# Performance work log

Measured on AMD Instinct MI355X. Metric: run time of the kernel, lower is better.

## Reference

```python
import jax, jax.numpy as jnp
import numpy as np
from jax import lax

DIM = 256
HEADS = 8
DIM_HEAD = 32
INNER = HEADS * DIM_HEAD  # 256
SCALE = DIM_HEAD ** -0.5
EPS = 1e-5
DN = ('NCHW', 'OIHW', 'NCHW')


def chan_layer_norm(x, g):
    # LayerNorm over channel dim (axis=1), biased variance
    mean = jnp.mean(x, axis=1, keepdims=True)
    var = jnp.mean((x - mean) ** 2, axis=1, keepdims=True)
    return (x - mean) / jnp.sqrt(var + EPS) * g


def conv1x1(x, w):
    return lax.conv_general_dilated(x, w, (1, 1), 'VALID', dimension_numbers=DN)


def dwconv3x3(x, w):
    # depthwise 3x3, padding=1, groups=channels; w: [C,1,3,3]
    return lax.conv_general_dilated(x, w, (1, 1), 'SAME', dimension_numbers=DN,
                                    feature_group_count=x.shape[1])


def setup_inputs() -> dict:
    key = jax.random.key(0)
    ks = jax.random.split(key, 9)
    B, X, Y = 16, 64, 64
    fmap = jax.random.normal(ks[0], (B, DIM, X, Y), dtype=jnp.float32)
    w = lambda k, shape: (jax.random.normal(k, shape, dtype=jnp.float32) * 0.02)
    return {
        'fmap': fmap,
        'g_norm': jnp.ones((1, DIM, 1, 1), dtype=jnp.float32),
        'wq1': w(ks[1], (INNER, DIM, 1, 1)),
        'wq_dw': w(ks[2], (INNER, 1, 3, 3)),
        'wk1': w(ks[3], (INNER, DIM, 1, 1)),
        'wk_dw': w(ks[4], (INNER, 1, 3, 3)),
        'wv1': w(ks[5], (INNER, DIM, 1, 1)),
        'wv_dw': w(ks[6], (INNER, 1, 3, 3)),
        'wo': w(ks[7], (DIM, INNER, 1, 1)),
        'g_out': jnp.ones((1, DIM, 1, 1), dtype=jnp.float32),
    }


def reference(fmap, g_norm, wq1, wq_dw, wk1, wk_dw, wv1, wv_dw, wo, g_out):
    b, _, X, Y = fmap.shape
    n = X * Y
    x = chan_layer_norm(fmap, g_norm)
    # QKV: 1x1 conv -> depthwise 3x3 conv (dropout is identity in eval)
    q = dwconv3x3(conv1x1(x, wq1), wq_dw)
    k = dwconv3x3(conv1x1(x, wk1), wk_dw)
    v = dwconv3x3(conv1x1(x, wv1), wv_dw)
    # b (h c) x y -> b h n c
    def split(t):
        return t.reshape(b, HEADS, DIM_HEAD, n).transpose(0, 1, 3, 2)
    q, k, v = split(q), split(k), split(v)
    q = jax.nn.softmax(q, axis=-1) * SCALE   # softmax over feature dim
    k = jax.nn.softmax(k, axis=-2)           # softmax over sequence dim
    ctx = jnp.einsum('bhnd,bhne->bhde', k, v)    # [b,h,d,d]
    out = jnp.einsum('bhnd,bhde->bhne', q, ctx)  # [b,h,n,d]
    # b h n d -> b (h d) x y
    out = out.transpose(0, 1, 3, 2).reshape(b, INNER, X, Y)
    out = jax.nn.silu(out)
    out = conv1x1(out, wo)
    return chan_layer_norm(out, g_out)
```

## Files before the change

### kernel.cpp

```cpp
#include <hip/hip_runtime.h>


typedef unsigned short u16;
typedef __bf16 bf16x8 __attribute__((ext_vector_type(8)));
typedef float f32x4 __attribute__((ext_vector_type(4)));
typedef float f32x16 __attribute__((ext_vector_type(16)));

#define DEV static __device__ __forceinline__

DEV float b2f(u16 u) { return __uint_as_float(((unsigned int)u) << 16); }
DEV u16 f2bf(float f) {
  unsigned int u = __float_as_uint(f);
  return (u16)((u + 0x7fffu + ((u >> 16) & 1u)) >> 16);
}
DEV void gl2lds16(const void* g, void* l) {
  __builtin_amdgcn_global_load_lds((__attribute__((address_space(1))) void*)g,
                                   (__attribute__((address_space(3))) void*)l, 16, 0, 0);
}

__global__ __launch_bounds__(256) void prep_kernel(const float* __restrict__ wk,
                                                   const float* __restrict__ wv,
                                                   const float* __restrict__ wq,
                                                   const float* __restrict__ wo,
                                                   u16* __restrict__ wb) {
  const int i = blockIdx.x * 256 + threadIdx.x;
  const float* src = (blockIdx.y == 0) ? wk : (blockIdx.y == 1) ? wv : (blockIdx.y == 2) ? wq : wo;
  wb[blockIdx.y * 65536 + i] = f2bf(src[i]);
}

__global__ __launch_bounds__(256) void ln_tin_kernel(const float* __restrict__ f,
                                                     const float* __restrict__ g,
                                                     u16* __restrict__ xT) {
  __shared__ u16 tile[64 * 258];
  __shared__ float red[2 * 256];
  __shared__ float mu_s[64], inv_s[64];
  const int t = threadIdx.x;
  const int p0 = blockIdx.x * 64;
  const int b = blockIdx.y;
  const long fb = (long)b * 256 * 4096;
  const int p = t & 63, cg = t >> 6;
  float s1 = 0.f, s2 = 0.f;
  for (int pass = 0; pass < 64; ++pass) {
    int c = pass * 4 + cg;
    float v = f[fb + (long)c * 4096 + p0 + p];
    s1 += v; s2 += v * v;
    tile[p * 258 + c] = f2bf(v);
  }
  red[cg * 64 + p] = s1;
  red[256 + cg * 64 + p] = s2;
  __syncthreads();
  if (t < 64) {
    float a1 = red[t] + red[64 + t] + red[128 + t] + red[192 + t];
    float a2 = red[256 + t] + red[320 + t] + red[384 + t] + red[448 + t];
    float mu = a1 * (1.f / 256.f);
    float var = a2 * (1.f / 256.f) - mu * mu;
    mu_s[t] = mu;
    inv_s[t] = 1.0f / sqrtf(var + 1e-5f);
  }
  __syncthreads();
  {
    float gc = g[t];
    for (int pp = 0; pp < 64; ++pp) {
      float v = b2f(tile[pp * 258 + t]);
      xT[((long)b * 4096 + p0 + pp) * 256 + t] = f2bf((v - mu_s[pp]) * inv_s[pp] * gc);
    }
  }
}

__global__ __launch_bounds__(256) void gemm_bt_kernel(
    const u16* __restrict__ A, const u16* __restrict__ B0, const u16* __restrict__ B1,
    u16* __restrict__ Cg, int ldc, long sA, long sC) {
  __shared__ u16 As[128 * 32];
  __shared__ u16 Bs[128 * 32];
  const int t = threadIdx.x;
  const int wave = t >> 6, lane = t & 63, quad = lane >> 4, l16 = lane & 15;
  const int wr = wave >> 1, wc = wave & 1;
  const int m0 = blockIdx.x * 128;
  const int jt = blockIdx.y;
  const int b = blockIdx.z;
  const u16* Ab = A + (long)b * sA + (long)m0 * 256;
  const u16* Bt = (jt < 2 ? B0 : B1) + (jt & 1) * 128 * 256;
  u16* Cb = Cg + (long)b * sC + (long)m0 * ldc + jt * 128;

  const int srow = lane >> 2;
  const int scol = (lane & 3) * 8;
  f32x4 acc[4][4];
#pragma unroll
  for (int i = 0; i < 4; ++i)
#pragma unroll
    for (int j = 0; j < 4; ++j) acc[i][j] = (f32x4){0.f, 0.f, 0.f, 0.f};

  const int aoff = (wr * 64 + l16) * 32 + quad * 8;
  const int boff = (wc * 64 + l16) * 32 + quad * 8;

  for (int ks = 0; ks < 8; ++ks) {
    const int k0 = ks * 32;
    __syncthreads();
    for (int i = wave; i < 8; i += 4) {
      gl2lds16(Ab + (i * 16 + srow) * 256 + k0 + scol, &As[i * 512 + lane * 8]);
      gl2lds16(Bt + (i * 16 + srow) * 256 + k0 + scol, &Bs[i * 512 + lane * 8]);
    }
    __syncthreads();
    bf16x8 af[4], bfr[4];
#pragma unroll
    for (int mt = 0; mt < 4; ++mt) af[mt] = *(const bf16x8*)&As[aoff + mt * 512];
#pragma unroll
    for (int nt = 0; nt < 4; ++nt) bfr[nt] = *(const bf16x8*)&Bs[boff + nt * 512];
#pragma unroll
    for (int mt = 0; mt < 4; ++mt)
#pragma unroll
      for (int nt = 0; nt < 4; ++nt)
        acc[mt][nt] = __builtin_amdgcn_mfma_f32_16x16x32_bf16(af[mt], bfr[nt], acc[mt][nt], 0, 0, 0);
  }
#pragma unroll
  for (int mt = 0; mt < 4; ++mt) {
    const int mbase = wr * 64 + mt * 16 + quad * 4;
#pragma unroll
    for (int nt = 0; nt < 4; ++nt) {
      const int n = wc * 64 + nt * 16 + l16;
#pragma unroll
      for (int r = 0; r < 4; ++r)
        Cb[(long)(mbase + r) * ldc + n] = f2bf(acc[mt][nt][r]);
    }
  }
}

__global__ __launch_bounds__(256) void dwq_kernel(const u16* __restrict__ qT,
                                                  const float* __restrict__ wdw,
                                                  u16* __restrict__ qp) {
  const int t = threadIdx.x;
  const int strip = blockIdx.x, h = blockIdx.y, b = blockIdx.z;
  const int x0 = strip * 4;
  const int wave = t >> 6, lane = t & 63;
  const int ysel = lane & 15, cg = lane >> 4;
  const int y = wave * 16 + ysel;
  float w[72];
#pragma unroll
  for (int q = 0; q < 8; ++q)
#pragma unroll
    for (int i = 0; i < 9; ++i) w[q * 9 + i] = wdw[(h * 32 + cg * 8 + q) * 9 + i];
  const u16* qb = qT + (long)b * 4096 * 256 + h * 32 + cg * 8;
  u16* ob = qp + ((long)b * 4096 + y) * 256 + h * 32 + cg * 8;

#pragma unroll
  for (int it = 0; it < 4; ++it) {
    const int x = x0 + it;
    float acc[8] = {0.f, 0.f, 0.f, 0.f, 0.f, 0.f, 0.f, 0.f};
#pragma unroll
    for (int r = 0; r < 3; ++r) {
      const int xx = x - 1 + r;
#pragma unroll
      for (int dy = 0; dy < 3; ++dy) {
        const int yy = y - 1 + dy;
        if (((unsigned)xx < 64u) & ((unsigned)yy < 64u)) {
          uint4 pk = *(const uint4*)(qb + (long)(xx * 64 + yy) * 256);
          const u16* s = (const u16*)&pk;
#pragma unroll
          for (int q = 0; q < 8; ++q)
            acc[q] = fmaf(w[q * 9 + r * 3 + dy], b2f(s[q]), acc[q]);
        }
      }
    }
    float e[8];
    float s = 0.f;
#pragma unroll
    for (int q = 0; q < 8; ++q) { e[q] = __expf(acc[q]); s += e[q]; }
    s += __shfl_xor(s, 16);
    s += __shfl_xor(s, 32);
    const float inv = 0.17677669529663687f / s;
    uint4 o;
    u16* os = (u16*)&o;
#pragma unroll
    for (int q = 0; q < 8; ++q) os[q] = f2bf(e[q] * inv);
    *(uint4*)(ob + (long)x * 16384) = o;
  }
}

__global__ __launch_bounds__(1024, 4) void ctx_kernel(const u16* __restrict__ kvT,
                                                      const float* __restrict__ wkdw,
                                                      const float* __restrict__ wvdw,
                                                      float* __restrict__ par0,
                                                      float* __restrict__ par1) {
  __shared__ float redb[8 * 1088];
  __shared__ float redk[16 * 32];
  const int t = threadIdx.x;
  const int strip = blockIdx.x, h = blockIdx.y, b = blockIdx.z;
  const int wave = t >> 6, lane = t & 63;
  const int g = wave >> 2, wq = wave & 3;
  const int x0 = strip * 32 + g * 8;
  const int c = lane & 31, half = lane >> 5;
  const int ystart = wq * 16 + half * 8;
  float wk[9], wv[9];
#pragma unroll
  for (int i = 0; i < 9; ++i) {
    wk[i] = wkdw[(h * 32 + c) * 9 + i];
    wv[i] = wvdw[(h * 32 + c) * 9 + i];
  }
  const u16* kb = kvT + (long)b * 4096 * 512 + h * 32 + c;

  float fk[3][10], fv[3][10];
#pragma unroll
  for (int r = 0; r < 2; ++r) {
    const int x = x0 - 1 + r;
#pragma unroll
    for (int m = 0; m < 10; ++m) {
      const int yy = ystart - 1 + m;
      float a = 0.f, bb = 0.f;
      if (((unsigned)x < 64u) & ((unsigned)yy < 64u)) {
        const u16* p = kb + (long)(x * 64 + yy) * 512;
        a = b2f(p[0]);
        bb = b2f(p[256]);
      }
      fk[r][m] = a; fv[r][m] = bb;
    }
  }
  f32x16 acc;
#pragma unroll
  for (int r = 0; r < 16; ++r) acc[r] = 0.f;
  float ks = 0.f;

  for (int it = 0; it < 8; ++it) {
    const int x = x0 + it;
    {
      const int xn = x + 1;
#pragma unroll
      for (int m = 0; m < 10; ++m) {
        const int yy = ystart - 1 + m;
        float a = 0.f, bb = 0.f;
        if (((unsigned)xn < 64u) & ((unsigned)yy < 64u)) {
          const u16* p = kb + (long)(xn * 64 + yy) * 512;
          a = b2f(p[0]);
          bb = b2f(p[256]);
        }
        fk[2][m] = a; fv[2][m] = bb;
      }
    }
    union { bf16x8 v; u16 s[8]; } af, bf_;
#pragma unroll
    for (int j = 0; j < 8; ++j) {
      float a = 0.f, bb = 0.f;
#pragma unroll
      for (int r = 0; r < 3; ++r)
#pragma unroll
        for (int dy = 0; dy < 3; ++dy) {
          a = fmaf(wk[r * 3 + dy], fk[r][j + dy], a);
          bb = fmaf(wv[r * 3 + dy], fv[r][j + dy], bb);
        }
      const u16 eb = f2bf(__expf(a));
      ks += b2f(eb);
      af.s[j] = eb;
      bf_.s[j] = f2bf(bb);
    }
    acc = __builtin_amdgcn_mfma_f32_32x32x16_bf16(af.v, bf_.v, acc, 0, 0, 0);
#pragma unroll
    for (int m = 0; m < 10; ++m) {
      fk[0][m] = fk[1][m]; fk[1][m] = fk[2][m];
      fv[0][m] = fv[1][m]; fv[1][m] = fv[2][m];
    }
  }
  ks += __shfl_xor(ks, 32);
  if (half == 0) redk[wave * 32 + c] = ks;
  if (wave >= 8) {
#pragma unroll
    for (int r = 0; r < 16; ++r) redb[(wave - 8) * 1088 + lane * 17 + r] = acc[r];
  }
  __syncthreads();
  if (wave < 8) {
#pragma unroll
    for (int r = 0; r < 16; ++r) acc[r] += redb[wave * 1088 + lane * 17 + r];
  }
  __syncthreads();
  if (wave >= 4 && wave < 8) {
#pragma unroll
    for (int r = 0; r < 16; ++r) redb[(wave - 4) * 1088 + lane * 17 + r] = acc[r];
  }
  __syncthreads();
  if (wave < 4) {
#pragma unroll
    for (int r = 0; r < 16; ++r) acc[r] += redb[wave * 1088 + lane * 17 + r];
  }
  __syncthreads();
  if (wave >= 1 && wave < 4) {
#pragma unroll
    for (int r = 0; r < 16; ++r) redb[(wave - 1) * 1088 + lane * 17 + r] = acc[r];
  }
  __syncthreads();
  if (wave == 0) {
    float* par = (strip ? par1 : par0) + (long)(b * 8 + h) * 1056;
#pragma unroll
    for (int r = 0; r < 16; ++r) {
      float sum = acc[r] + redb[lane * 17 + r] + redb[1088 + lane * 17 + r] +
                  redb[2176 + lane * 17 + r];
      const int d = (r & 3) + 8 * (r >> 2) + 4 * half;
      par[d * 32 + c] = sum;
    }
    if (t < 32) {
      float s = 0.f;
#pragma unroll
      for (int w = 0; w < 16; ++w) s += redk[w * 32 + t];
      par[1024 + t] = s;
    }
  }
}

__global__ __launch_bounds__(256) void reduce_kernel(const float* __restrict__ par0,
                                                     const float* __restrict__ par1,
                                                     float* __restrict__ ctxF,
                                                     float* __restrict__ ksF) {
  const int bh = blockIdx.x;
  const long base = (long)bh * 1056;
  for (int i = threadIdx.x; i < 1056; i += 256) {
    float v = par0[base + i] + par1[base + i];
    if (i < 1024) ctxF[(long)bh * 1024 + i] = v;
    else ksF[(long)bh * 32 + (i - 1024)] = v;
  }
}

__global__ __launch_bounds__(256) void attn_kernel(const u16* __restrict__ qp,
                                                   const float* __restrict__ ctxg,
                                                   const float* __restrict__ ksumg,
                                                   u16* __restrict__ sout) {
  __shared__ u16 cnhi[8 * 32 * 40];
  __shared__ u16 cnlo[8 * 32 * 40];
  const int t = threadIdx.x;
  const int p0 = blockIdx.x * 128;
  const int b = blockIdx.y;
  const int wave = t >> 6, lane = t & 63, quad = lane >> 4, l16 = lane & 15;

  for (int j = 0; j < 32; ++j) {
    const int idx = j * 256 + t;
    const int e = idx & 31, d = (idx >> 5) & 31, h = idx >> 10;
    const float c = ctxg[(long)b * 8192 + idx] / ksumg[(long)b * 256 + (idx >> 5)];
    const u16 hi = f2bf(c);
    cnhi[h * 1280 + e * 40 + d] = hi;
    cnlo[h * 1280 + e * 40 + d] = f2bf(c - b2f(hi));
  }
  __syncthreads();

  const u16* qb = qp + ((long)b * 4096 + p0 + wave * 32) * 256;
  u16* ob = sout + ((long)b * 4096 + p0 + wave * 32) * 256;
#pragma unroll
  for (int h = 0; h < 8; ++h) {
    const int cb = h * 1280 + quad * 8;
    const bf16x8 bhi0 = *(const bf16x8*)&cnhi[cb + l16 * 40];
    const bf16x8 bhi1 = *(const bf16x8*)&cnhi[cb + (16 + l16) * 40];
    const bf16x8 blo0 = *(const bf16x8*)&cnlo[cb + l16 * 40];
    const bf16x8 blo1 = *(const bf16x8*)&cnlo[cb + (16 + l16) * 40];
#pragma unroll
    for (int rt = 0; rt < 2; ++rt) {
      const bf16x8 af = *(const bf16x8*)&qb[(rt * 16 + l16) * 256 + h * 32 + quad * 8];
      f32x4 a0 = (f32x4){0.f, 0.f, 0.f, 0.f};
      f32x4 a1 = (f32x4){0.f, 0.f, 0.f, 0.f};
      a0 = __builtin_amdgcn_mfma_f32_16x16x32_bf16(af, blo0, a0, 0, 0, 0);
      a0 = __builtin_amdgcn_mfma_f32_16x16x32_bf16(af, bhi0, a0, 0, 0, 0);
      a1 = __builtin_amdgcn_mfma_f32_16x16x32_bf16(af, blo1, a1, 0, 0, 0);
      a1 = __builtin_amdgcn_mfma_f32_16x16x32_bf16(af, bhi1, a1, 0, 0, 0);
#pragma unroll
      for (int r = 0; r < 4; ++r) {
        const int row = rt * 16 + quad * 4 + r;
        const float v0 = a0[r], v1 = a1[r];
        ob[(long)row * 256 + h * 32 + l16] = f2bf(v0 / (1.f + __expf(-v0)));
        ob[(long)row * 256 + h * 32 + 16 + l16] = f2bf(v1 / (1.f + __expf(-v1)));
      }
    }
  }
}

__global__ __launch_bounds__(256) void ln_tout_kernel(const u16* __restrict__ y,
                                                      const float* __restrict__ gout,
                                                      float* __restrict__ out) {
  __shared__ u16 tile[64 * 258];
  __shared__ float red[2 * 256];
  __shared__ float mu_s[64], inv_s[64];
  const int t = threadIdx.x;
  const int p0 = blockIdx.x * 64;
  const int b = blockIdx.y;
  for (int p = 0; p < 64; ++p)
    tile[p * 258 + t] = y[((long)b * 4096 + p0 + p) * 256 + t];
  __syncthreads();
  {
    const int p = t & 63, part = t >> 6;
    float s1 = 0.f, s2 = 0.f;
    for (int k = 0; k < 64; ++k) {
      float v = b2f(tile[p * 258 + part * 64 + k]);
      s1 += v; s2 += v * v;
    }
    red[part * 64 + p] = s1;
    red[256 + part * 64 + p] = s2;
  }
  __syncthreads();
  if (t < 64) {
    float s1 = red[t] + red[64 + t] + red[128 + t] + red[192 + t];
    float s2 = red[256 + t] + red[320 + t] + red[384 + t] + red[448 + t];
    float mu = s1 * (1.f / 256.f);
    float var = s2 * (1.f / 256.f) - mu * mu;
    mu_s[t] = mu;
    inv_s[t] = 1.0f / sqrtf(var + 1e-5f);
  }
  __syncthreads();
  {
    const int p = t & 63, cg = t >> 6;
    const long ob = (long)b * 256 * 4096;
    for (int pass = 0; pass < 64; ++pass) {
      int c = pass * 4 + cg;
      float v = b2f(tile[p * 258 + c]);
      out[ob + (long)c * 4096 + p0 + p] = (v - mu_s[p]) * inv_s[p] * gout[c];
    }
  }
}

extern "C" void kernel_launch(void* const* d_in, const int* in_sizes, int n_in,
                              void* d_out, int out_size, void* d_ws, size_t ws_size,
                              hipStream_t stream) {
  (void)in_sizes; (void)n_in; (void)out_size; (void)ws_size;
  const float* fmap = (const float*)d_in[0];
  const float* gnorm = (const float*)d_in[1];
  const float* wq1 = (const float*)d_in[2];
  const float* wqdw = (const float*)d_in[3];
  const float* wk1 = (const float*)d_in[4];
  const float* wkdw = (const float*)d_in[5];
  const float* wv1 = (const float*)d_in[6];
  const float* wvdw = (const float*)d_in[7];
  const float* wo = (const float*)d_in[8];
  const float* gout = (const float*)d_in[9];
  float* out = (float*)d_out;
  char* ws = (char*)d_ws;

  float* par0 = (float*)(ws);
  u16* wb = (u16*)(ws + 540672);
  float* par1 = (float*)(ws + 1064960);
  u16* wk_bf = wb;
  u16* wv_bf = wb + 65536;
  u16* wq_bf = wb + 131072;
  u16* wo_bf = wb + 196608;
  u16* xT = (u16*)(ws + 2097152);
  u16* kvT = (u16*)(ws + 35651584);
  u16* qT = kvT;
  float* ctxF = (float*)(ws + 35651584);
  float* ksF = (float*)(ws + 35651584 + 524288);
  u16* qp = (u16*)(ws + 69206016);
  u16* sbuf = xT;
  u16* ybuf = qp;

  prep_kernel<<<dim3(256, 4), 256, 0, stream>>>(wk1, wv1, wq1, wo, wb);
  ln_tin_kernel<<<dim3(64, 16), 256, 0, stream>>>(fmap, gnorm, xT);
  gemm_bt_kernel<<<dim3(32, 4, 16), 256, 0, stream>>>(xT, wk_bf, wv_bf, kvT, 512,
                                                      4096L * 256, 4096L * 512);
  ctx_kernel<<<dim3(2, 8, 16), 1024, 0, stream>>>(kvT, wkdw, wvdw, par0, par1);
  gemm_bt_kernel<<<dim3(32, 2, 16), 256, 0, stream>>>(xT, wq_bf, wq_bf, qT, 256,
                                                      4096L * 256, 4096L * 256);
  dwq_kernel<<<dim3(16, 8, 16), 256, 0, stream>>>(qT, wqdw, qp);
  reduce_kernel<<<dim3(128), 256, 0, stream>>>(par0, par1, ctxF, ksF);
  attn_kernel<<<dim3(32, 16), 256, 0, stream>>>(qp, ctxF, ksF, sbuf);
  gemm_bt_kernel<<<dim3(32, 2, 16), 256, 0, stream>>>(sbuf, wo_bf, wo_bf, ybuf, 256,
                                                      4096L * 256, 4096L * 256);
  ln_tout_kernel<<<dim3(64, 16), 256, 0, stream>>>(ybuf, gout, out);
}
```

Measured before the change: 327.9 us.

## Interleave K/V channels, stage dwq halo tile in LDS, split attn by head pairs

The K and V projection weights are interleaved row-wise so the GEMM writes K and V channels side by side. This lets ctx_kernel fetch both with a single 32-bit load instead of two strided 16-bit loads. dwq_kernel now stages a 6-row halo tile of q in shared memory, so the 3x3 stencil reads LDS rather than issuing nine bounds-checked global loads per output. attn_kernel gains a grid dimension over head pairs, which cuts per-block LDS and context setup and increases the block count, at the cost of re-reading q rows in smaller per-head slices.

```diff
diff --git a/kernel.cpp b/kernel.cpp
--- a/kernel.cpp
+++ b/kernel.cpp
@@ -24,8 +24,11 @@
                                                    const float* __restrict__ wo,
                                                    u16* __restrict__ wb) {
   const int i = blockIdx.x * 256 + threadIdx.x;
-  const float* src = (blockIdx.y == 0) ? wk : (blockIdx.y == 1) ? wv : (blockIdx.y == 2) ? wq : wo;
-  wb[blockIdx.y * 65536 + i] = f2bf(src[i]);
+  const int yb = blockIdx.y;
+  if (yb == 0)      wb[(i >> 8) * 512 + (i & 255)] = f2bf(wk[i]);
+  else if (yb == 1) wb[(i >> 8) * 512 + 256 + (i & 255)] = f2bf(wv[i]);
+  else if (yb == 2) wb[131072 + i] = f2bf(wq[i]);
+  else              wb[196608 + i] = f2bf(wo[i]);
 }
 
 __global__ __launch_bounds__(256) void ln_tin_kernel(const float* __restrict__ f,
@@ -128,37 +131,48 @@
 __global__ __launch_bounds__(256) void dwq_kernel(const u16* __restrict__ qT,
                                                   const float* __restrict__ wdw,
                                                   u16* __restrict__ qp) {
+  __shared__ u16 tile[6 * 66 * 40];
   const int t = threadIdx.x;
   const int strip = blockIdx.x, h = blockIdx.y, b = blockIdx.z;
   const int x0 = strip * 4;
   const int wave = t >> 6, lane = t & 63;
   const int ysel = lane & 15, cg = lane >> 4;
   const int y = wave * 16 + ysel;
+  const int ty = t >> 2, tc = t & 3;
+
+  if (t < 48) {
+    const int slot = t >> 3, brd = (t >> 2) & 1, c4 = t & 3;
+    *(uint4*)&tile[slot * 2640 + (brd ? 65 * 40 : 0) + c4 * 8] = (uint4){0, 0, 0, 0};
+  }
+  const u16* qrow = qT + (long)b * 4096 * 256 + h * 32 + tc * 8;
+#pragma unroll
+  for (int s = 0; s < 6; ++s) {
+    const int xx = x0 - 1 + s;
+    uint4 v = (uint4){0, 0, 0, 0};
+    if ((unsigned)xx < 64u) v = *(const uint4*)(qrow + (long)(xx * 64 + ty) * 256);
+    *(uint4*)&tile[s * 2640 + (ty + 1) * 40 + tc * 8] = v;
+  }
   float w[72];
 #pragma unroll
   for (int q = 0; q < 8; ++q)
 #pragma unroll
     for (int i = 0; i < 9; ++i) w[q * 9 + i] = wdw[(h * 32 + cg * 8 + q) * 9 + i];
-  const u16* qb = qT + (long)b * 4096 * 256 + h * 32 + cg * 8;
+  __syncthreads();
+
   u16* ob = qp + ((long)b * 4096 + y) * 256 + h * 32 + cg * 8;
-
 #pragma unroll
   for (int it = 0; it < 4; ++it) {
     const int x = x0 + it;
     float acc[8] = {0.f, 0.f, 0.f, 0.f, 0.f, 0.f, 0.f, 0.f};
 #pragma unroll
     for (int r = 0; r < 3; ++r) {
-      const int xx = x - 1 + r;
 #pragma unroll
       for (int dy = 0; dy < 3; ++dy) {
-        const int yy = y - 1 + dy;
-        if (((unsigned)xx < 64u) & ((unsigned)yy < 64u)) {
-          uint4 pk = *(const uint4*)(qb + (long)(xx * 64 + yy) * 256);
-          const u16* s = (const u16*)&pk;
-#pragma unroll
-          for (int q = 0; q < 8; ++q)
-            acc[q] = fmaf(w[q * 9 + r * 3 + dy], b2f(s[q]), acc[q]);
-        }
+        uint4 pk = *(const uint4*)&tile[(it + r) * 2640 + (y + dy) * 40 + cg * 8];
+        const u16* s = (const u16*)&pk;
+#pragma unroll
+        for (int q = 0; q < 8; ++q)
+          acc[q] = fmaf(w[q * 9 + r * 3 + dy], b2f(s[q]), acc[q]);
       }
     }
     float e[8];
@@ -196,7 +210,7 @@
     wk[i] = wkdw[(h * 32 + c) * 9 + i];
     wv[i] = wvdw[(h * 32 + c) * 9 + i];
   }
-  const u16* kb = kvT + (long)b * 4096 * 512 + h * 32 + c;
+  const u16* kb = kvT + (long)b * 4096 * 512 + 2 * (h * 32 + c);
 
   float fk[3][10], fv[3][10];
 #pragma unroll
@@ -207,9 +221,9 @@
       const int yy = ystart - 1 + m;
       float a = 0.f, bb = 0.f;
       if (((unsigned)x < 64u) & ((unsigned)yy < 64u)) {
-        const u16* p = kb + (long)(x * 64 + yy) * 512;
-        a = b2f(p[0]);
-        bb = b2f(p[256]);
+        const unsigned u = *(const unsigned*)(kb + (long)(x * 64 + yy) * 512);
+        a = b2f((u16)(u & 0xffffu));
+        bb = b2f((u16)(u >> 16));
       }
       fk[r][m] = a; fv[r][m] = bb;
     }
@@ -228,9 +242,9 @@
         const int yy = ystart - 1 + m;
         float a = 0.f, bb = 0.f;
         if (((unsigned)xn < 64u) & ((unsigned)yy < 64u)) {
-          const u16* p = kb + (long)(xn * 64 + yy) * 512;
-          a = b2f(p[0]);
-          bb = b2f(p[256]);
+          const unsigned u = *(const unsigned*)(kb + (long)(xn * 64 + yy) * 512);
+          a = b2f((u16)(u & 0xffffu));
+          bb = b2f((u16)(u >> 16));
         }
         fk[2][m] = a; fv[2][m] = bb;
       }
@@ -320,28 +334,31 @@
                                                    const float* __restrict__ ctxg,
                                                    const float* __restrict__ ksumg,
                                                    u16* __restrict__ sout) {
-  __shared__ u16 cnhi[8 * 32 * 40];
-  __shared__ u16 cnlo[8 * 32 * 40];
+  __shared__ u16 cnhi[2 * 32 * 40];
+  __shared__ u16 cnlo[2 * 32 * 40];
   const int t = threadIdx.x;
   const int p0 = blockIdx.x * 128;
-  const int b = blockIdx.y;
+  const int hp = blockIdx.y;
+  const int b = blockIdx.z;
   const int wave = t >> 6, lane = t & 63, quad = lane >> 4, l16 = lane & 15;
 
-  for (int j = 0; j < 32; ++j) {
-    const int idx = j * 256 + t;
-    const int e = idx & 31, d = (idx >> 5) & 31, h = idx >> 10;
-    const float c = ctxg[(long)b * 8192 + idx] / ksumg[(long)b * 256 + (idx >> 5)];
+  for (int j = 0; j < 8; ++j) {
+    const int lidx = j * 256 + t;
+    const int e = lidx & 31, d = (lidx >> 5) & 31, hh = lidx >> 10;
+    const int gd = (hp * 2 + hh) * 32 + d;
+    const float c = ctxg[(long)b * 8192 + gd * 32 + e] / ksumg[(long)b * 256 + gd];
     const u16 hi = f2bf(c);
-    cnhi[h * 1280 + e * 40 + d] = hi;
-    cnlo[h * 1280 + e * 40 + d] = f2bf(c - b2f(hi));
+    cnhi[hh * 1280 + e * 40 + d] = hi;
+    cnlo[hh * 1280 + e * 40 + d] = f2bf(c - b2f(hi));
   }
   __syncthreads();
 
   const u16* qb = qp + ((long)b * 4096 + p0 + wave * 32) * 256;
   u16* ob = sout + ((long)b * 4096 + p0 + wave * 32) * 256;
 #pragma unroll
-  for (int h = 0; h < 8; ++h) {
-    const int cb = h * 1280 + quad * 8;
+  for (int hh = 0; hh < 2; ++hh) {
+    const int h = hp * 2 + hh;
+    const int cb = hh * 1280 + quad * 8;
     const bf16x8 bhi0 = *(const bf16x8*)&cnhi[cb + l16 * 40];
     const bf16x8 bhi1 = *(const bf16x8*)&cnhi[cb + (16 + l16) * 40];
     const bf16x8 blo0 = *(const bf16x8*)&cnlo[cb + l16 * 40];
@@ -429,8 +446,7 @@
   float* par0 = (float*)(ws);
   u16* wb = (u16*)(ws + 540672);
   float* par1 = (float*)(ws + 1064960);
-  u16* wk_bf = wb;
-  u16* wv_bf = wb + 65536;
+  u16* wkv_bf = wb;
   u16* wq_bf = wb + 131072;
   u16* wo_bf = wb + 196608;
   u16* xT = (u16*)(ws + 2097152);
@@ -444,14 +460,14 @@
 
   prep_kernel<<<dim3(256, 4), 256, 0, stream>>>(wk1, wv1, wq1, wo, wb);
   ln_tin_kernel<<<dim3(64, 16), 256, 0, stream>>>(fmap, gnorm, xT);
-  gemm_bt_kernel<<<dim3(32, 4, 16), 256, 0, stream>>>(xT, wk_bf, wv_bf, kvT, 512,
+  gemm_bt_kernel<<<dim3(32, 4, 16), 256, 0, stream>>>(xT, wkv_bf, wkv_bf + 65536, kvT, 512,
                                                       4096L * 256, 4096L * 512);
   ctx_kernel<<<dim3(2, 8, 16), 1024, 0, stream>>>(kvT, wkdw, wvdw, par0, par1);
   gemm_bt_kernel<<<dim3(32, 2, 16), 256, 0, stream>>>(xT, wq_bf, wq_bf, qT, 256,
                                                       4096L * 256, 4096L * 256);
   dwq_kernel<<<dim3(16, 8, 16), 256, 0, stream>>>(qT, wqdw, qp);
   reduce_kernel<<<dim3(128), 256, 0, stream>>>(par0, par1, ctxF, ksF);
-  attn_kernel<<<dim3(32, 16), 256, 0, stream>>>(qp, ctxF, ksF, sbuf);
+  attn_kernel<<<dim3(32, 4, 16), 256, 0, stream>>>(qp, ctxF, ksF, sbuf);
   gemm_bt_kernel<<<dim3(32, 2, 16), 256, 0, stream>>>(sbuf, wo_bf, wo_bf, ybuf, 256,
                                                       4096L * 256, 4096L * 256);
   ln_tout_kernel<<<dim3(64, 16), 256, 0, stream>>>(ybuf, gout, out);
```

Result: no change. 321.7 us (-1.9%).
